# Optimization experiments

Measured on AMD Instinct MI355X. Metric: run time of the kernel, lower is better.

The kernel has to match this reference:

```python
import jax, jax.numpy as jnp
import numpy as np

DIM = 192
HEADS = 4
HID = int(DIM * 2.66)  # 510, Restormer GDFN hidden dim
EPS_LN = 1e-6


def ln2d(x, w, b):
    # torch LayerNorm2d variant: global mean/std over (C,H,W), std is UNBIASED (ddof=1)
    n = x.shape[1] * x.shape[2] * x.shape[3]
    mean = x.mean(axis=(1, 2, 3), keepdims=True)
    var = ((x - mean) ** 2).sum(axis=(1, 2, 3), keepdims=True) / (n - 1)
    return (x - mean) / (jnp.sqrt(var) + EPS_LN) * w + b


def conv1x1(x, w):
    # w: [O, C]; pointwise conv as channel matmul
    return jnp.einsum('bchw,oc->bohw', x, w)


def dwconv3(x, w):
    # w: [C, 1, 3, 3] depthwise 3x3, padding=1
    return jax.lax.conv_general_dilated(
        x, w, window_strides=(1, 1), padding='SAME',
        dimension_numbers=('NCHW', 'OIHW', 'NCHW'),
        feature_group_count=x.shape[1])


def setup_inputs() -> dict:
    key = jax.random.key(0)
    ks = jax.random.split(key, 8)
    s = 0.02
    return {
        'x': jax.random.normal(ks[0], (2, DIM, 256, 256), dtype=jnp.float32),
        'n1_w': jnp.ones((1, DIM, 1, 1), jnp.float32),
        'n1_b': jnp.zeros((1, DIM, 1, 1), jnp.float32),
        'qkv_w': jax.random.normal(ks[1], (3 * DIM, DIM), jnp.float32) * s,
        'qkv_dw_w': jax.random.normal(ks[2], (3 * DIM, 1, 3, 3), jnp.float32) * s,
        'proj_w': jax.random.normal(ks[3], (DIM, DIM), jnp.float32) * s,
        'temperature': jnp.ones((HEADS, 1, 1), jnp.float32),
        'n2_w': jnp.ones((1, DIM, 1, 1), jnp.float32),
        'n2_b': jnp.zeros((1, DIM, 1, 1), jnp.float32),
        'ff_in_w': jax.random.normal(ks[4], (2 * HID, DIM), jnp.float32) * s,
        'ff_dw_w': jax.random.normal(ks[5], (2 * HID, 1, 3, 3), jnp.float32) * s,
        'ff_out_w': jax.random.normal(ks[6], (DIM, HID), jnp.float32) * s,
    }


def reference(x, n1_w, n1_b, qkv_w, qkv_dw_w, proj_w, temperature,
              n2_w, n2_b, ff_in_w, ff_dw_w, ff_out_w):
    b, c, h, w = x.shape
    hd = c // HEADS

    # ---- MDTA attention ----
    y = ln2d(x, n1_w, n1_b)
    qkv = dwconv3(conv1x1(y, qkv_w), qkv_dw_w)  # [b, 3c, h, w]
    q, k, v = jnp.split(qkv, 3, axis=1)
    q = q.reshape(b, HEADS, hd, h * w)
    k = k.reshape(b, HEADS, hd, h * w)
    v = v.reshape(b, HEADS, hd, h * w)
    # L2-normalize along spatial axis (F.normalize, eps=1e-12)
    q = q / jnp.maximum(jnp.linalg.norm(q, axis=-1, keepdims=True), 1e-12)
    k = k / jnp.maximum(jnp.linalg.norm(k, axis=-1, keepdims=True), 1e-12)
    attn = jnp.einsum('bhcn,bhdn->bhcd', q, k) * temperature  # [b,H,hd,hd]
    attn = jax.nn.softmax(attn, axis=-1)
    out = jnp.einsum('bhcd,bhdn->bhcn', attn, v).reshape(b, c, h, w)
    x = x + conv1x1(out, proj_w)

    # ---- GDFN feed-forward ----
    y = ln2d(x, n2_w, n2_b)
    y = dwconv3(conv1x1(y, ff_in_w), ff_dw_w)  # [b, 2*HID, h, w]
    x1, x2 = jnp.split(y, 2, axis=1)
    y = jax.nn.gelu(x1, approximate=False) * x2
    x = x + conv1x1(y, ff_out_w)
    return x
```

## Files before the change

kernel.cpp:

```cpp
#include <hip/hip_runtime.h>
#include <hip/hip_bf16.h>

typedef unsigned short u16;
typedef __attribute__((ext_vector_type(8))) short short8;
typedef __attribute__((ext_vector_type(8))) unsigned short ushort8v;
typedef __attribute__((ext_vector_type(4))) float f32x4;

#define NPIX  65536
#define HH    256
#define WW    256
#define BATCH 2
#define CDIM  192
#define NHEADS 4
#define HD    48
#define OQKV  576
#define HIDN  510
#define OPAD  1024
#define NSLOT 32

__device__ __forceinline__ float bf2f(u16 b) {
  union { unsigned u; float f; } v; v.u = ((unsigned)b) << 16; return v.f;
}
__device__ __forceinline__ u16 f2bf(float f) {
  __bf16 h = (__bf16)f;
  u16 r; __builtin_memcpy(&r, &h, 2); return r;
}
__device__ __forceinline__ void atomAddF(float* p, float v) { unsafeAtomicAdd(p, v); }
__device__ __forceinline__ void gload16(const void* g, void* l) {
  __builtin_amdgcn_global_load_lds((const __attribute__((address_space(1))) unsigned int*)g,
                                   (__attribute__((address_space(3))) unsigned int*)l, 16, 0, 0);
}
__device__ __forceinline__ void xcdswz(int& bx, int& by) {
  const int nx = gridDim.x;
  const int tot = nx * gridDim.y;
  const int lin = by * nx + bx;
  const int q = tot >> 3, r = tot & 7;
  const int xcd = lin & 7, pos = lin >> 3;
  const int nl = (xcd < r) ? (xcd * (q + 1) + pos) : (r * (q + 1) + (xcd - r) * q + pos);
  bx = nl % nx; by = nl / nx;
}
__device__ __forceinline__ void dw3row(const u16* __restrict__ rp, int jm, bool hasL, bool hasR,
                                       float w0, float w1, float w2, float* acc) {
  ushort8v m = *(const ushort8v*)(rp + jm);
  float f[10];
  f[0] = hasL ? bf2f(rp[jm - 1]) : 0.f;
  #pragma unroll
  for (int t = 0; t < 8; ++t) f[t + 1] = bf2f(m[t]);
  f[9] = hasR ? bf2f(rp[jm + 8]) : 0.f;
  #pragma unroll
  for (int i = 0; i < 8; ++i) acc[i] += w0 * f[i] + w1 * f[i + 1] + w2 * f[i + 2];
}

#define OFF_STATS1 ((size_t)0)
#define OFF_STATS2 ((size_t)512)
#define OFF_G      ((size_t)1024)
#define OFF_NQ     (OFF_G + 2359296)
#define OFF_NK     (OFF_NQ + 49152)
#define ZERO_BYTES (OFF_NK + 49152)
#define OFF_BQ     ZERO_BYTES
#define OFF_B2     (OFF_BQ + 4608)
#define OFF_M      (OFF_B2 + 8192)
#define OFF_WQ     (OFF_M + 294912)
#define OFF_W2B    (OFF_WQ + 442368)
#define OFF_W3     (OFF_W2B + 786432)
#define OFF_T      (OFF_W3 + 196608)
#define OFF_QKV    (OFF_T + 50331648)
#define OFF_BAND   (OFF_QKV + 150994944)

__global__ __launch_bounds__(256) void k_statsT(const float* __restrict__ P, u16* __restrict__ T,
                                                float* __restrict__ stats) {
  __shared__ u16 ld[128][200];
  const int b = blockIdx.y, n0 = blockIdx.x * 128, tid = threadIdx.x;
  const int slot = blockIdx.x & (NSLOT - 1);
  const float* Pb = P + (((size_t)b * CDIM) << 16) + n0;
  float s = 0.f, ss = 0.f;
  for (int it = 0; it < 24; ++it) {
    int idx = it * 256 + tid;
    int c = idx >> 5, j = idx & 31;
    float4 v = *(const float4*)(Pb + ((size_t)c << 16) + j * 4);
    s  += v.x + v.y + v.z + v.w;
    ss += v.x*v.x + v.y*v.y + v.z*v.z + v.w*v.w;
    int px = j * 4;
    ld[px][c] = f2bf(v.x); ld[px+1][c] = f2bf(v.y);
    ld[px+2][c] = f2bf(v.z); ld[px+3][c] = f2bf(v.w);
  }
  for (int off = 32; off; off >>= 1) { s += __shfl_down(s, off); ss += __shfl_down(ss, off); }
  __shared__ float ls[4], lss[4];
  const int wid = tid >> 6, lane = tid & 63;
  if (lane == 0) { ls[wid] = s; lss[wid] = ss; }
  __syncthreads();
  if (tid == 0) {
    atomAddF(&stats[(slot * BATCH + b) * 2 + 0], ls[0]+ls[1]+ls[2]+ls[3]);
    atomAddF(&stats[(slot * BATCH + b) * 2 + 1], lss[0]+lss[1]+lss[2]+lss[3]);
  }
  u16* Tb = T + (size_t)(b * NPIX + n0) * CDIM;
  for (int it = 0; it < 12; ++it) {
    int idx = it * 256 + tid;
    int ch = idx % 24, nl = idx / 24;
    union { u16 s[8]; uint4 v; } t;
    #pragma unroll
    for (int r = 0; r < 8; ++r) t.s[r] = ld[nl][ch * 8 + r];
    int sch = ch ^ (nl & 7);
    *(uint4*)((char*)(Tb + (size_t)nl * CDIM) + sch * 16) = t.v;
  }
}

__global__ void k_fold(const float* __restrict__ w_in, const float* __restrict__ ln_w,
                       const float* __restrict__ ln_b, const float* __restrict__ stats,
                       u16* __restrict__ W, float* __restrict__ bias, int O_real) {
  const int o = blockIdx.x, b = blockIdx.y, c = threadIdx.x;
  const int Mtot = gridDim.x;
  const float n = (float)(CDIM * NPIX);
  float sum = 0.f, sumsq = 0.f;
  for (int sl = 0; sl < NSLOT; ++sl) {
    sum   += stats[(sl * BATCH + b) * 2 + 0];
    sumsq += stats[(sl * BATCH + b) * 2 + 1];
  }
  const float mean = sum / n;
  const float var = (sumsq - sum * sum / n) / (n - 1.f);
  const float inv = 1.f / (sqrtf(var) + 1e-6f);
  float we = 0.f, cb = 0.f;
  if (o < O_real) {
    float wi = w_in[o * CDIM + c];
    float a  = ln_w[c] * inv;
    we = wi * a;
    cb = wi * (ln_b[c] - mean * a);
  }
  int sch = (c >> 3) ^ (o & 7);
  W[((size_t)b * Mtot + o) * CDIM + sch * 8 + (c & 7)] = f2bf(we);
  for (int off = 32; off; off >>= 1) cb += __shfl_down(cb, off);
  __shared__ float l[3];
  if ((threadIdx.x & 63) == 0) l[threadIdx.x >> 6] = cb;
  __syncthreads();
  if (threadIdx.x == 0) bias[b * Mtot + o] = l[0] + l[1] + l[2];
}

__global__ void k_fold3(const float* __restrict__ w, u16* __restrict__ W3) {
  const int o = blockIdx.x;
  for (int it = 0; it < 2; ++it) {
    int c = it * 256 + threadIdx.x;
    float v = (c < HIDN) ? w[o * HIDN + c] : 0.f;
    int sch = (c >> 3) ^ (o & 7);
    W3[o * 512 + sch * 8 + (c & 7)] = f2bf(v);
  }
}

template <int KTOT, int KC, int EPI, int STATS, int NT>
__global__ __launch_bounds__(256) void k_mgemm(
    const u16* __restrict__ Bm, const u16* __restrict__ Am,
    const float* __restrict__ bias,
    const u16* __restrict__ rT, long rTbstr,
    void* __restrict__ outv, long Obstr, int out_nstr,
    u16* __restrict__ tout, long toutbstr,
    int Mtot, long Bbstr, long Abstr,
    int nB_base, int nB_rows, int nO_base, float* __restrict__ stats)
{
  constexpr int RBC = KC * 2;
  constexpr int NFR = NT / 64;
  constexpr int LDSB = (NT + 64) * KC * 2;
  constexpr int EPIB = (EPI == 0) ? 64 * (NT + 8) * 2
                     : (EPI == 2) ? 128 * 66 * 4
                     : ((EPI == 3) ? 128 * 66 * 2 : 0);
  constexpr int TOT  = LDSB > EPIB ? LDSB : EPIB;
  __shared__ char lds[TOT];
  u16* lB = (u16*)lds;
  u16* lA = (u16*)(lds + NT * KC * 2);
  const int b = blockIdx.z;
  int bx = blockIdx.x, by = blockIdx.y;
  xcdswz(bx, by);
  const int o0 = bx * 64;
  const int nB = nB_base + by * NT;
  const int nO = nO_base + by * NT;
  const int tid = threadIdx.x;
  const int lane = tid & 63;
  const int wid = tid >> 6;

  if (EPI == 0 && (nB < 0 || nB >= nB_rows)) {
    u16* op = (u16*)outv;
    uint4 z; z.x = z.y = z.z = z.w = 0u;
    constexpr int CH8 = NT / 8;
    #pragma unroll
    for (int it = 0; it < NT / 32; ++it) {
      int idx = it * 256 + tid;
      int orow = idx / CH8, c8 = idx % CH8;
      *(uint4*)(op + (size_t)b * Obstr + (size_t)(o0 + orow) * out_nstr + nO + c8 * 8) = z;
    }
    return;
  }

  const u16* Bb = Bm + (size_t)b * Bbstr + (size_t)nB * KTOT;
  const u16* Ab = Am + (size_t)b * Abstr + (size_t)o0 * KTOT;

  f32x4 acc[4][NFR];
  #pragma unroll
  for (int m = 0; m < 4; ++m)
    #pragma unroll
    for (int nf = 0; nf < NFR; ++nf) acc[m][nf] = (f32x4){0.f, 0.f, 0.f, 0.f};

  for (int kc0 = 0; kc0 < KTOT; kc0 += KC) {
    if (kc0) __syncthreads();
    constexpr int NCH = KC / 8;
    #pragma unroll
    for (int it = 0; it < NT * NCH / 256; ++it) {
      int idx = it * 256 + tid; int r = idx / NCH, ch = idx % NCH;
      gload16((const char*)(Bb + (size_t)r * KTOT + kc0) + ch * 16, (char*)lB + idx * 16);
    }
    #pragma unroll
    for (int it = 0; it < 64 * NCH / 256; ++it) {
      int idx = it * 256 + tid; int r = idx / NCH, ch = idx % NCH;
      gload16((const char*)(Ab + (size_t)r * KTOT + kc0) + ch * 16, (char*)lA + idx * 16);
    }
    __syncthreads();
    const int lr = lane & 15, g = lane >> 4;
    #pragma unroll
    for (int ks = 0; ks < KC / 32; ++ks) {
      const int ck = ks * 4 + g;
      short8 afr[4], bfr[NFR];
      #pragma unroll
      for (int m = 0; m < 4; ++m) {
        int row = m * 16 + lr;
        afr[m] = *(const short8*)((const char*)lA + row * RBC + ((ck ^ (row & 7)) << 4));
      }
      #pragma unroll
      for (int nf = 0; nf < NFR; ++nf) {
        int row = wid * (NT / 4) + nf * 16 + lr;
        bfr[nf] = *(const short8*)((const char*)lB + row * RBC + ((ck ^ (row & 7)) << 4));
      }
      #pragma unroll
      for (int m = 0; m < 4; ++m)
        #pragma unroll
        for (int nf = 0; nf < NFR; ++nf)
          acc[m][nf] = __builtin_amdgcn_mfma_f32_16x16x32_bf16(afr[m], bfr[nf], acc[m][nf], 0, 0, 0);
    }
  }

  const int col = lane & 15, rg = lane >> 4;
  if constexpr (EPI == 0) {
    constexpr int NTP = NT + 8;
    u16* lst = (u16*)lds;
    __syncthreads();
    #pragma unroll
    for (int m = 0; m < 4; ++m)
      #pragma unroll
      for (int j = 0; j < 4; ++j) {
        int r = m * 16 + rg * 4 + j;
        float bv = bias[b * Mtot + o0 + r];
        #pragma unroll
        for (int nf = 0; nf < NFR; ++nf) {
          int nn = wid * (NT / 4) + nf * 16 + col;
          lst[r * NTP + nn] = f2bf(acc[m][nf][j] + bv);
        }
      }
    __syncthreads();
    u16* op = (u16*)outv;
    constexpr int CH8 = NT / 8;
    #pragma unroll
    for (int it = 0; it < 64 * CH8 / 256; ++it) {
      int idx = it * 256 + tid;
      int r = idx / CH8, ch = idx % CH8;
      uint4 v = *(const uint4*)(lst + r * NTP + ch * 8);
      *(uint4*)(op + (size_t)b * Obstr + (size_t)(o0 + r) * out_nstr + nO + ch * 8) = v;
    }
  } else if constexpr (EPI == 2) {
    float* lBf = (float*)lds;
    __syncthreads();
    #pragma unroll
    for (int m = 0; m < 4; ++m)
      #pragma unroll
      for (int nf = 0; nf < NFR; ++nf)
        #pragma unroll
        for (int j = 0; j < 4; ++j)
          lBf[(wid * 32 + nf * 16 + col) * 66 + m * 16 + rg * 4 + j] = acc[m][nf][j];
    __syncthreads();
    float s = 0.f, ss = 0.f;
    for (int it = 0; it < 4; ++it) {
      int idx = it * 256 + tid;
      int n = idx >> 3, ch3 = idx & 7;
      size_t rowoff = (size_t)(nO + n) * CDIM;
      int chunk = (o0 >> 3) + (ch3 ^ (n & 7));
      uint4 xv = *(const uint4*)((const char*)(rT + (size_t)b * rTbstr + rowoff) + chunk * 16);
      u16* xs = (u16*)&xv;
      union { u16 s[8]; uint4 v; } t;
      #pragma unroll
      for (int r = 0; r < 8; ++r) {
        float rv = bf2f(xs[r]) + lBf[n * 66 + ch3 * 8 + r];
        t.s[r] = f2bf(rv);
        if constexpr (STATS) { s += rv; ss += rv * rv; }
      }
      *(uint4*)((char*)(tout + (size_t)b * toutbstr + rowoff) + chunk * 16) = t.v;
    }
    if constexpr (STATS) {
      for (int off = 32; off; off >>= 1) { s += __shfl_down(s, off); ss += __shfl_down(ss, off); }
      __shared__ float sr1[4], sr2[4];
      if (lane == 0) { sr1[wid] = s; sr2[wid] = ss; }
      __syncthreads();
      if (tid == 0) {
        int slot = by & (NSLOT - 1);
        atomAddF(&stats[(slot * BATCH + b) * 2 + 0], sr1[0]+sr1[1]+sr1[2]+sr1[3]);
        atomAddF(&stats[(slot * BATCH + b) * 2 + 1], sr2[0]+sr2[1]+sr2[2]+sr2[3]);
      }
    }
  } else {
    u16* lAx = (u16*)lds;
    __syncthreads();
    for (int it = 0; it < 4; ++it) {
      int idx = it * 256 + tid;
      int n = idx >> 3, ch3 = idx & 7;
      int chunk = (o0 >> 3) + (ch3 ^ (n & 7));
      uint4 xv = *(const uint4*)((const char*)(rT + (size_t)b * rTbstr + (size_t)(nO + n) * CDIM) + chunk * 16);
      u16* xs = (u16*)&xv;
      #pragma unroll
      for (int r = 0; r < 8; ++r) lAx[n * 66 + ch3 * 8 + r] = xs[r];
    }
    __syncthreads();
    float* of = (float*)outv;
    #pragma unroll
    for (int m = 0; m < 4; ++m)
      #pragma unroll
      for (int nf = 0; nf < NFR; ++nf)
        #pragma unroll
        for (int j = 0; j < 4; ++j) {
          int o = o0 + m * 16 + rg * 4 + j;
          int nl = wid * 32 + nf * 16 + col;
          size_t ix = (size_t)b * Obstr + (size_t)o * out_nstr + nO + nl;
          of[ix] = acc[m][nf][j] + bf2f(lAx[nl * 66 + m * 16 + rg * 4 + j]);
        }
  }
}

__global__ __launch_bounds__(256) void k_gram(const u16* __restrict__ qkv,
                                              const float* __restrict__ dww,
                                              float* __restrict__ G,
                                              float* __restrict__ nq,
                                              float* __restrict__ nk) {
  __shared__ u16 qs[HD][128], ks2[HD][128];
  __shared__ u16 wq[HD][9], wk[HD][9];
  __shared__ float nql[HD], nkl[HD];
  int bx = blockIdx.x, by = blockIdx.y;
  xcdswz(bx, by);
  const int b = by >> 2, h = by & 3;
  const int row = bx >> 1, col0 = (bx & 1) * 128;
  const int slot = bx & (NSLOT - 1);
  const int bh = b * NHEADS + h;
  const int tid = threadIdx.x;

  for (int idx = tid; idx < HD * 9; idx += 256) {
    int c = idx / 9, k9 = idx % 9;
    wq[c][k9] = f2bf(dww[(h * HD + c) * 9 + k9]);
    wk[c][k9] = f2bf(dww[(CDIM + h * HD + c) * 9 + k9]);
  }
  __syncthreads();

  for (int it = 0; it < 6; ++it) {
    int idx = it * 256 + tid;
    int j = idx & 15, cz = idx >> 4;
    int c = cz % HD, qk = cz / HD;
    const u16* base = qkv + (((size_t)(b * OQKV + qk * CDIM + h * HD + c)) << 16);
    const u16* w = qk ? wk[c] : wq[c];
    float acc[8] = {0.f,0.f,0.f,0.f,0.f,0.f,0.f,0.f};
    const int jm = col0 + j * 8;
    const bool hasL = jm > 0, hasR = jm < 248;
    if (row > 0)   dw3row(base + (row - 1) * 256, jm, hasL, hasR, bf2f(w[0]), bf2f(w[1]), bf2f(w[2]), acc);
                   dw3row(base + row * 256,       jm, hasL, hasR, bf2f(w[3]), bf2f(w[4]), bf2f(w[5]), acc);
    if (row < 255) dw3row(base + (row + 1) * 256, jm, hasL, hasR, bf2f(w[6]), bf2f(w[7]), bf2f(w[8]), acc);
    union { u16 s[8]; ushort8v v; } rv;
    float sqs = 0.f;
    #pragma unroll
    for (int i = 0; i < 8; ++i) {
      rv.s[i] = f2bf(acc[i]);
      sqs += acc[i] * acc[i];
    }
    const int sw = (j ^ (c & 7)) * 8;
    if (qk) *(ushort8v*)&ks2[c][sw] = rv.v;
    else    *(ushort8v*)&qs[c][sw]  = rv.v;
    sqs += __shfl_down(sqs, 8);
    sqs += __shfl_down(sqs, 4);
    sqs += __shfl_down(sqs, 2);
    sqs += __shfl_down(sqs, 1);
    if ((tid & 15) == 0) { if (qk) nkl[c] = sqs; else nql[c] = sqs; }
  }
  __syncthreads();

  if (tid < HD) atomAddF(&nq[(slot * 2 * NHEADS + bh) * HD + tid], nql[tid]);
  else if (tid < 2*HD) atomAddF(&nk[(slot * 2 * NHEADS + bh) * HD + tid - HD], nkl[tid - HD]);

  const int lane = tid & 63, wid = tid >> 6;
  const int lr = lane & 15, g = lane >> 4;
  float* Gb = G + (size_t)(slot * 2 * NHEADS + bh) * HD * HD;
  for (int t = wid; t < 9; t += 4) {
    const int m = t / 3, nb = t % 3;
    f32x4 a4 = (f32x4){0.f, 0.f, 0.f, 0.f};
    #pragma unroll
    for (int ksi = 0; ksi < 4; ++ksi) {
      int ck = ksi * 4 + g;
      int ra = m * 16 + lr, rb = nb * 16 + lr;
      short8 af = *(const short8*)&qs[ra][(ck ^ (ra & 7)) * 8];
      short8 bf = *(const short8*)&ks2[rb][(ck ^ (rb & 7)) * 8];
      a4 = __builtin_amdgcn_mfma_f32_16x16x32_bf16(af, bf, a4, 0, 0, 0);
    }
    #pragma unroll
    for (int jj = 0; jj < 4; ++jj)
      atomAddF(&Gb[(m * 16 + g * 4 + jj) * HD + nb * 16 + lr], a4[jj]);
  }
}

__global__ void k_attnM(const float* __restrict__ G, const float* __restrict__ nq,
                        const float* __restrict__ nk, const float* __restrict__ temp,
                        const float* __restrict__ proj_w, u16* __restrict__ Mb16) {
  const int h = blockIdx.x, b = blockIdx.y;
  const int bh = b * NHEADS + h;
  __shared__ float at[HD][HD];
  __shared__ float nqs[HD], nks[HD];
  const int tid = threadIdx.x;
  if (tid < HD) {
    float s = 0.f;
    for (int sl = 0; sl < NSLOT; ++sl) s += nq[(sl * 2 * NHEADS + bh) * HD + tid];
    nqs[tid] = fmaxf(sqrtf(s), 1e-12f);
  } else if (tid >= 64 && tid < 64 + HD) {
    int c = tid - 64;
    float s = 0.f;
    for (int sl = 0; sl < NSLOT; ++sl) s += nk[(sl * 2 * NHEADS + bh) * HD + c];
    nks[c] = fmaxf(sqrtf(s), 1e-12f);
  }
  __syncthreads();
  const float t = temp[h];
  for (int idx = tid; idx < HD * HD; idx += 256) {
    int c = idx / HD, d = idx % HD;
    float g = 0.f;
    for (int sl = 0; sl < NSLOT; ++sl)
      g += G[(size_t)(sl * 2 * NHEADS + bh) * HD * HD + idx];
    at[c][d] = g / (nqs[c] * nks[d]) * t;
  }
  __syncthreads();
  if (tid < HD) {
    float m = -1e30f;
    for (int d = 0; d < HD; ++d) m = fmaxf(m, at[tid][d]);
    float s = 0.f;
    for (int d = 0; d < HD; ++d) { float e = __expf(at[tid][d] - m); at[tid][d] = e; s += e; }
    float inv = 1.f / s;
    for (int d = 0; d < HD; ++d) at[tid][d] *= inv;
  }
  __syncthreads();
  for (int idx = tid; idx < CDIM * HD; idx += 256) {
    int o = idx / HD, d = idx % HD;
    float acc = 0.f;
    for (int c = 0; c < HD; ++c) acc += proj_w[o * CDIM + h * HD + c] * at[c][d];
    int cf = h * HD + d;
    int sch = (cf >> 3) ^ (o & 7);
    Mb16[((size_t)(b * CDIM + o)) * CDIM + sch * 8 + (cf & 7)] = f2bf(acc);
  }
}

__global__ __launch_bounds__(256) void k_dwT(const u16* __restrict__ qkv,
                                             const float* __restrict__ dww,
                                             u16* __restrict__ vdwT, long vdwbstr) {
  __shared__ u16 ld[64][201];
  __shared__ float w9[CDIM][9];
  int bx = blockIdx.x, by = blockIdx.y;
  xcdswz(bx, by);
  const int b = by;
  const int p0 = bx * 64;
  const int row = p0 >> 8, col0 = p0 & 255;
  const int tid = threadIdx.x;
  for (int idx = tid; idx < CDIM * 9; idx += 256) w9[idx / 9][idx % 9] = dww[384 * 9 + idx];
  __syncthreads();
  for (int it = 0; it < 6; ++it) {
    int idx = it * 256 + tid;
    int j = idx & 7, c = idx >> 3;
    const u16* base = qkv + (((size_t)(b * OQKV + 384 + c)) << 16);
    const float* w = w9[c];
    float acc[8] = {0.f,0.f,0.f,0.f,0.f,0.f,0.f,0.f};
    const int jm = col0 + j * 8;
    const bool hasL = jm > 0, hasR = jm < 248;
    if (row > 0)   dw3row(base + (row - 1) * 256, jm, hasL, hasR, w[0], w[1], w[2], acc);
                   dw3row(base + row * 256,       jm, hasL, hasR, w[3], w[4], w[5], acc);
    if (row < 255) dw3row(base + (row + 1) * 256, jm, hasL, hasR, w[6], w[7], w[8], acc);
    #pragma unroll
    for (int i = 0; i < 8; ++i) ld[j * 8 + i][c] = f2bf(acc[i]);
  }
  __syncthreads();
  u16* Tb = vdwT + (size_t)b * vdwbstr + (size_t)p0 * CDIM;
  for (int it = 0; it < 6; ++it) {
    int idx = it * 256 + tid;
    int ch = idx % 24, pl = idx / 24;
    union { u16 s[8]; uint4 v; } t;
    #pragma unroll
    for (int r = 0; r < 8; ++r) t.s[r] = ld[pl][ch * 8 + r];
    int sch = ch ^ (pl & 7);
    *(uint4*)((char*)(Tb + (size_t)pl * CDIM) + sch * 16) = t.v;
  }
}

__global__ __launch_bounds__(256) void k_dwgT(const u16* __restrict__ hp_, const float* __restrict__ w9,
                                              u16* __restrict__ ygT, int rows_loc, int band_px) {
  __shared__ u16 ld[32][515];
  int bx = blockIdx.x, by = blockIdx.y;
  xcdswz(bx, by);
  const int b = by;
  const int p0 = bx * 32;
  const int olr = p0 >> 8, col0 = p0 & 255;
  const int tid = threadIdx.x;
  if (tid < 64) {
    int px = tid >> 1, c = 510 + (tid & 1);
    ld[px][c] = 0;
  }
  __syncthreads();
  for (int it = 0; it < 8; ++it) {
    int idx = it * 256 + tid;
    if (idx >= HIDN * 4) break;
    int j = idx & 3, c = idx >> 2;
    const u16* ia = hp_ + (size_t)(b * OPAD + c) * rows_loc * 256;
    const u16* ig = hp_ + (size_t)(b * OPAD + c + HIDN) * rows_loc * 256;
    float aa[8] = {0.f,0.f,0.f,0.f,0.f,0.f,0.f,0.f};
    float gg[8] = {0.f,0.f,0.f,0.f,0.f,0.f,0.f,0.f};
    const int jm = col0 + j * 8;
    const bool hasL = jm > 0, hasR = jm < 248;
    #pragma unroll
    for (int dr = 0; dr < 3; ++dr) {
      dw3row(ia + (olr + dr) * 256, jm, hasL, hasR,
             w9[c * 9 + dr * 3], w9[c * 9 + dr * 3 + 1], w9[c * 9 + dr * 3 + 2], aa);
      dw3row(ig + (olr + dr) * 256, jm, hasL, hasR,
             w9[(c + HIDN) * 9 + dr * 3], w9[(c + HIDN) * 9 + dr * 3 + 1],
             w9[(c + HIDN) * 9 + dr * 3 + 2], gg);
    }
    #pragma unroll
    for (int i = 0; i < 8; ++i) {
      float a = aa[i];
      float gel = 0.5f * a * (1.f + erff(a * 0.70710678118654752f));
      ld[j * 8 + i][c] = f2bf(gel * gg[i]);
    }
  }
  __syncthreads();
  u16* Tb = ygT + ((size_t)b * band_px + p0) * 512;
  for (int it = 0; it < 8; ++it) {
    int idx = it * 256 + tid;
    int ch = idx & 63, pl = idx >> 6;
    union { u16 s[8]; uint4 v; } t;
    #pragma unroll
    for (int r = 0; r < 8; ++r) t.s[r] = ld[pl][ch * 8 + r];
    int sch = ch ^ (pl & 7);
    *(uint4*)((char*)(Tb + (size_t)pl * 512) + sch * 16) = t.v;
  }
}

extern "C" void kernel_launch(void* const* d_in, const int* in_sizes, int n_in,
                              void* d_out, int out_size, void* d_ws, size_t ws_size,
                              hipStream_t stream) {
  const float* x       = (const float*)d_in[0];
  const float* n1_w    = (const float*)d_in[1];
  const float* n1_b    = (const float*)d_in[2];
  const float* qkv_w   = (const float*)d_in[3];
  const float* qkv_dw  = (const float*)d_in[4];
  const float* proj_w  = (const float*)d_in[5];
  const float* temp    = (const float*)d_in[6];
  const float* n2_w    = (const float*)d_in[7];
  const float* n2_b    = (const float*)d_in[8];
  const float* ff_in_w = (const float*)d_in[9];
  const float* ff_dw   = (const float*)d_in[10];
  const float* ff_out_w= (const float*)d_in[11];

  char* ws = (char*)d_ws;
  float* stats1 = (float*)(ws + OFF_STATS1);
  float* stats2 = (float*)(ws + OFF_STATS2);
  float* G      = (float*)(ws + OFF_G);
  float* nq     = (float*)(ws + OFF_NQ);
  float* nk     = (float*)(ws + OFF_NK);
  float* biasq  = (float*)(ws + OFF_BQ);
  float* bias2  = (float*)(ws + OFF_B2);
  u16*   Mb16   = (u16*)(ws + OFF_M);
  u16*   Wq     = (u16*)(ws + OFF_WQ);
  u16*   W2b    = (u16*)(ws + OFF_W2B);
  u16*   W3     = (u16*)(ws + OFF_W3);
  u16*   xT     = (u16*)(ws + OFF_T);
  u16*   qkv    = (u16*)(ws + OFF_QKV);
  u16*   vdwT   = qkv;
  u16*   x2T    = qkv + (size_t)CDIM * NPIX;
  const long qkvbstr = (long)OQKV * NPIX;
  float* outp   = (float*)d_out;

  int NP = 32;
  const int cand[4] = {2, 4, 8, 16};
  for (int i = 0; i < 4; ++i) {
    int rws = 256 / cand[i], rl = rws + 2;
    size_t band = (size_t)2 * OPAD * rl * 256 * 2 + (size_t)2 * rws * 256 * 512 * 2;
    if (OFF_BAND + band + ((size_t)8 << 20) <= ws_size) { NP = cand[i]; break; }
  }
  const int rows = 256 / NP, rows_loc = rows + 2, band_px = rows * 256;
  u16* hpre = (u16*)(ws + OFF_BAND);
  u16* ygT  = (u16*)(ws + OFF_BAND + (size_t)2 * OPAD * rows_loc * 256 * 2);

  hipMemsetAsync(ws, 0, ZERO_BYTES, stream);

  k_statsT<<<dim3(NPIX / 128, BATCH), 256, 0, stream>>>(x, xT, stats1);
  k_fold<<<dim3(OQKV, BATCH), CDIM, 0, stream>>>(qkv_w, n1_w, n1_b, stats1, Wq, biasq, OQKV);
  k_mgemm<192, 64, 0, 0, 256><<<dim3(OQKV / 64, NPIX / 256, BATCH), 256, 0, stream>>>(
      xT, Wq, biasq, nullptr, 0L, qkv, (long)OQKV * NPIX, NPIX, nullptr, 0L,
      OQKV, (long)NPIX * CDIM, (long)OQKV * CDIM, 0, NPIX, 0, nullptr);
  k_gram<<<dim3(512, BATCH * NHEADS), 256, 0, stream>>>(qkv, qkv_dw, G, nq, nk);
  k_attnM<<<dim3(NHEADS, BATCH), 256, 0, stream>>>(G, nq, nk, temp, proj_w, Mb16);
  k_dwT<<<dim3(NPIX / 64, BATCH), 256, 0, stream>>>(qkv, qkv_dw, vdwT, qkvbstr);
  k_mgemm<192, 64, 2, 1, 128><<<dim3(CDIM / 64, NPIX / 128, BATCH), 256, 0, stream>>>(
      vdwT, Mb16, nullptr, xT, (long)NPIX * CDIM, nullptr, 0L, 0, x2T, qkvbstr,
      CDIM, qkvbstr, (long)CDIM * CDIM, 0, NPIX, 0, stats2);

  k_fold<<<dim3(OPAD, BATCH), CDIM, 0, stream>>>(ff_in_w, n2_w, n2_b, stats2, W2b, bias2, 1020);
  k_fold3<<<dim3(CDIM), 256, 0, stream>>>(ff_out_w, W3);
  for (int rp = 0; rp < NP; ++rp) {
    const int band0 = rp * band_px;
    k_mgemm<192, 64, 0, 0, 256><<<dim3(OPAD / 64, rows_loc, BATCH), 256, 0, stream>>>(
        x2T, W2b, bias2, nullptr, 0L, hpre, (long)OPAD * rows_loc * 256, rows_loc * 256,
        nullptr, 0L, OPAD, qkvbstr, (long)OPAD * CDIM, band0 - 256, NPIX, 0, nullptr);
    k_dwgT<<<dim3(band_px / 32, BATCH), 256, 0, stream>>>(hpre, ff_dw, ygT, rows_loc, band_px);
    k_mgemm<512, 128, 3, 0, 128><<<dim3(CDIM / 64, rows * 2, BATCH), 256, 0, stream>>>(
        ygT, W3, nullptr, x2T, qkvbstr, outp, (long)CDIM * NPIX, NPIX, nullptr, 0L,
        CDIM, (long)band_px * 512, 0L, 0, band_px, band0, nullptr);
  }
}
```

Baseline: 750.4 us.

## Halve per-block tiles in depthwise/gram kernels and coalesce final GEMM stores

The final output GEMM epilogue now stages residual-added fp32 results through LDS, then writes them as coalesced float4 rows instead of scattered scalar stores. k_gram, k_dwT and k_dwgT each process half as many pixels per block, and twice as many blocks are launched, to raise occupancy and parallelism. k_gram uses a shorter K loop, and k_dwT stores its weights as bf16 in LDS. The costs are an extra LDS round trip and barriers in the epilogue, more per-block overhead, and twice as many atomic adds into the gram slots.

```diff
diff --git a/kernel.cpp b/kernel.cpp
--- a/kernel.cpp
+++ b/kernel.cpp
@@ -160,7 +160,7 @@
   constexpr int LDSB = (NT + 64) * KC * 2;
   constexpr int EPIB = (EPI == 0) ? 64 * (NT + 8) * 2
                      : (EPI == 2) ? 128 * 66 * 4
-                     : ((EPI == 3) ? 128 * 66 * 2 : 0);
+                     : ((EPI == 3) ? 64 * 132 * 4 : 0);
   constexpr int TOT  = LDSB > EPIB ? LDSB : EPIB;
   __shared__ char lds[TOT];
   u16* lB = (u16*)lds;
@@ -313,18 +313,33 @@
       for (int r = 0; r < 8; ++r) lAx[n * 66 + ch3 * 8 + r] = xs[r];
     }
     __syncthreads();
-    float* of = (float*)outv;
     #pragma unroll
     for (int m = 0; m < 4; ++m)
       #pragma unroll
       for (int nf = 0; nf < NFR; ++nf)
         #pragma unroll
         for (int j = 0; j < 4; ++j) {
-          int o = o0 + m * 16 + rg * 4 + j;
           int nl = wid * 32 + nf * 16 + col;
-          size_t ix = (size_t)b * Obstr + (size_t)o * out_nstr + nO + nl;
-          of[ix] = acc[m][nf][j] + bf2f(lAx[nl * 66 + m * 16 + rg * 4 + j]);
+          acc[m][nf][j] += bf2f(lAx[nl * 66 + m * 16 + rg * 4 + j]);
         }
+    __syncthreads();
+    float* lstf = (float*)lds;
+    #pragma unroll
+    for (int m = 0; m < 4; ++m)
+      #pragma unroll
+      for (int nf = 0; nf < NFR; ++nf)
+        #pragma unroll
+        for (int j = 0; j < 4; ++j)
+          lstf[(m * 16 + rg * 4 + j) * 132 + wid * 32 + nf * 16 + col] = acc[m][nf][j];
+    __syncthreads();
+    float* of = (float*)outv;
+    #pragma unroll
+    for (int it = 0; it < 8; ++it) {
+      int idx = it * 256 + tid;
+      int r = idx >> 5, q4 = idx & 31;
+      float4 v = *(const float4*)&lstf[r * 132 + q4 * 4];
+      *(float4*)(of + (size_t)b * Obstr + (size_t)(o0 + r) * out_nstr + nO + q4 * 4) = v;
+    }
   }
 }
 
@@ -333,13 +348,13 @@
                                               float* __restrict__ G,
                                               float* __restrict__ nq,
                                               float* __restrict__ nk) {
-  __shared__ u16 qs[HD][128], ks2[HD][128];
+  __shared__ u16 qs[HD][64], ks2[HD][64];
   __shared__ u16 wq[HD][9], wk[HD][9];
   __shared__ float nql[HD], nkl[HD];
   int bx = blockIdx.x, by = blockIdx.y;
   xcdswz(bx, by);
   const int b = by >> 2, h = by & 3;
-  const int row = bx >> 1, col0 = (bx & 1) * 128;
+  const int row = bx >> 2, col0 = (bx & 3) * 64;
   const int slot = bx & (NSLOT - 1);
   const int bh = b * NHEADS + h;
   const int tid = threadIdx.x;
@@ -351,9 +366,9 @@
   }
   __syncthreads();
 
-  for (int it = 0; it < 6; ++it) {
+  for (int it = 0; it < 3; ++it) {
     int idx = it * 256 + tid;
-    int j = idx & 15, cz = idx >> 4;
+    int j = idx & 7, cz = idx >> 3;
     int c = cz % HD, qk = cz / HD;
     const u16* base = qkv + (((size_t)(b * OQKV + qk * CDIM + h * HD + c)) << 16);
     const u16* w = qk ? wk[c] : wq[c];
@@ -373,11 +388,10 @@
     const int sw = (j ^ (c & 7)) * 8;
     if (qk) *(ushort8v*)&ks2[c][sw] = rv.v;
     else    *(ushort8v*)&qs[c][sw]  = rv.v;
-    sqs += __shfl_down(sqs, 8);
     sqs += __shfl_down(sqs, 4);
     sqs += __shfl_down(sqs, 2);
     sqs += __shfl_down(sqs, 1);
-    if ((tid & 15) == 0) { if (qk) nkl[c] = sqs; else nql[c] = sqs; }
+    if ((tid & 7) == 0) { if (qk) nkl[c] = sqs; else nql[c] = sqs; }
   }
   __syncthreads();
 
@@ -391,7 +405,7 @@
     const int m = t / 3, nb = t % 3;
     f32x4 a4 = (f32x4){0.f, 0.f, 0.f, 0.f};
     #pragma unroll
-    for (int ksi = 0; ksi < 4; ++ksi) {
+    for (int ksi = 0; ksi < 2; ++ksi) {
       int ck = ksi * 4 + g;
       int ra = m * 16 + lr, rb = nb * 16 + lr;
       short8 af = *(const short8*)&qs[ra][(ck ^ (ra & 7)) * 8];
@@ -454,61 +468,61 @@
 __global__ __launch_bounds__(256) void k_dwT(const u16* __restrict__ qkv,
                                              const float* __restrict__ dww,
                                              u16* __restrict__ vdwT, long vdwbstr) {
-  __shared__ u16 ld[64][201];
-  __shared__ float w9[CDIM][9];
-  int bx = blockIdx.x, by = blockIdx.y;
-  xcdswz(bx, by);
-  const int b = by;
-  const int p0 = bx * 64;
-  const int row = p0 >> 8, col0 = p0 & 255;
-  const int tid = threadIdx.x;
-  for (int idx = tid; idx < CDIM * 9; idx += 256) w9[idx / 9][idx % 9] = dww[384 * 9 + idx];
-  __syncthreads();
-  for (int it = 0; it < 6; ++it) {
-    int idx = it * 256 + tid;
-    int j = idx & 7, c = idx >> 3;
-    const u16* base = qkv + (((size_t)(b * OQKV + 384 + c)) << 16);
-    const float* w = w9[c];
-    float acc[8] = {0.f,0.f,0.f,0.f,0.f,0.f,0.f,0.f};
-    const int jm = col0 + j * 8;
-    const bool hasL = jm > 0, hasR = jm < 248;
-    if (row > 0)   dw3row(base + (row - 1) * 256, jm, hasL, hasR, w[0], w[1], w[2], acc);
-                   dw3row(base + row * 256,       jm, hasL, hasR, w[3], w[4], w[5], acc);
-    if (row < 255) dw3row(base + (row + 1) * 256, jm, hasL, hasR, w[6], w[7], w[8], acc);
-    #pragma unroll
-    for (int i = 0; i < 8; ++i) ld[j * 8 + i][c] = f2bf(acc[i]);
-  }
-  __syncthreads();
-  u16* Tb = vdwT + (size_t)b * vdwbstr + (size_t)p0 * CDIM;
-  for (int it = 0; it < 6; ++it) {
-    int idx = it * 256 + tid;
-    int ch = idx % 24, pl = idx / 24;
-    union { u16 s[8]; uint4 v; } t;
-    #pragma unroll
-    for (int r = 0; r < 8; ++r) t.s[r] = ld[pl][ch * 8 + r];
-    int sch = ch ^ (pl & 7);
-    *(uint4*)((char*)(Tb + (size_t)pl * CDIM) + sch * 16) = t.v;
-  }
-}
-
-__global__ __launch_bounds__(256) void k_dwgT(const u16* __restrict__ hp_, const float* __restrict__ w9,
-                                              u16* __restrict__ ygT, int rows_loc, int band_px) {
-  __shared__ u16 ld[32][515];
+  __shared__ u16 ld[32][201];
+  __shared__ u16 w9[CDIM][9];
   int bx = blockIdx.x, by = blockIdx.y;
   xcdswz(bx, by);
   const int b = by;
   const int p0 = bx * 32;
+  const int row = p0 >> 8, col0 = p0 & 255;
+  const int tid = threadIdx.x;
+  for (int idx = tid; idx < CDIM * 9; idx += 256) w9[idx / 9][idx % 9] = f2bf(dww[384 * 9 + idx]);
+  __syncthreads();
+  for (int it = 0; it < 3; ++it) {
+    int idx = it * 256 + tid;
+    int j = idx & 3, c = idx >> 2;
+    const u16* base = qkv + (((size_t)(b * OQKV + 384 + c)) << 16);
+    const u16* w = w9[c];
+    float acc[8] = {0.f,0.f,0.f,0.f,0.f,0.f,0.f,0.f};
+    const int jm = col0 + j * 8;
+    const bool hasL = jm > 0, hasR = jm < 248;
+    if (row > 0)   dw3row(base + (row - 1) * 256, jm, hasL, hasR, bf2f(w[0]), bf2f(w[1]), bf2f(w[2]), acc);
+                   dw3row(base + row * 256,       jm, hasL, hasR, bf2f(w[3]), bf2f(w[4]), bf2f(w[5]), acc);
+    if (row < 255) dw3row(base + (row + 1) * 256, jm, hasL, hasR, bf2f(w[6]), bf2f(w[7]), bf2f(w[8]), acc);
+    #pragma unroll
+    for (int i = 0; i < 8; ++i) ld[j * 8 + i][c] = f2bf(acc[i]);
+  }
+  __syncthreads();
+  u16* Tb = vdwT + (size_t)b * vdwbstr + (size_t)p0 * CDIM;
+  for (int it = 0; it < 3; ++it) {
+    int idx = it * 256 + tid;
+    int ch = idx % 24, pl = idx / 24;
+    union { u16 s[8]; uint4 v; } t;
+    #pragma unroll
+    for (int r = 0; r < 8; ++r) t.s[r] = ld[pl][ch * 8 + r];
+    int sch = ch ^ (pl & 7);
+    *(uint4*)((char*)(Tb + (size_t)pl * CDIM) + sch * 16) = t.v;
+  }
+}
+
+__global__ __launch_bounds__(256) void k_dwgT(const u16* __restrict__ hp_, const float* __restrict__ w9,
+                                              u16* __restrict__ ygT, int rows_loc, int band_px) {
+  __shared__ u16 ld[16][515];
+  int bx = blockIdx.x, by = blockIdx.y;
+  xcdswz(bx, by);
+  const int b = by;
+  const int p0 = bx * 16;
   const int olr = p0 >> 8, col0 = p0 & 255;
   const int tid = threadIdx.x;
-  if (tid < 64) {
+  if (tid < 32) {
     int px = tid >> 1, c = 510 + (tid & 1);
     ld[px][c] = 0;
   }
   __syncthreads();
-  for (int it = 0; it < 8; ++it) {
+  for (int it = 0; it < 4; ++it) {
     int idx = it * 256 + tid;
-    if (idx >= HIDN * 4) break;
-    int j = idx & 3, c = idx >> 2;
+    if (idx >= HIDN * 2) break;
+    int j = idx & 1, c = idx >> 1;
     const u16* ia = hp_ + (size_t)(b * OPAD + c) * rows_loc * 256;
     const u16* ig = hp_ + (size_t)(b * OPAD + c + HIDN) * rows_loc * 256;
     float aa[8] = {0.f,0.f,0.f,0.f,0.f,0.f,0.f,0.f};
@@ -532,7 +546,7 @@
   }
   __syncthreads();
   u16* Tb = ygT + ((size_t)b * band_px + p0) * 512;
-  for (int it = 0; it < 8; ++it) {
+  for (int it = 0; it < 4; ++it) {
     int idx = it * 256 + tid;
     int ch = idx & 63, pl = idx >> 6;
     union { u16 s[8]; uint4 v; } t;
@@ -596,9 +610,9 @@
   k_mgemm<192, 64, 0, 0, 256><<<dim3(OQKV / 64, NPIX / 256, BATCH), 256, 0, stream>>>(
       xT, Wq, biasq, nullptr, 0L, qkv, (long)OQKV * NPIX, NPIX, nullptr, 0L,
       OQKV, (long)NPIX * CDIM, (long)OQKV * CDIM, 0, NPIX, 0, nullptr);
-  k_gram<<<dim3(512, BATCH * NHEADS), 256, 0, stream>>>(qkv, qkv_dw, G, nq, nk);
+  k_gram<<<dim3(1024, BATCH * NHEADS), 256, 0, stream>>>(qkv, qkv_dw, G, nq, nk);
   k_attnM<<<dim3(NHEADS, BATCH), 256, 0, stream>>>(G, nq, nk, temp, proj_w, Mb16);
-  k_dwT<<<dim3(NPIX / 64, BATCH), 256, 0, stream>>>(qkv, qkv_dw, vdwT, qkvbstr);
+  k_dwT<<<dim3(NPIX / 32, BATCH), 256, 0, stream>>>(qkv, qkv_dw, vdwT, qkvbstr);
   k_mgemm<192, 64, 2, 1, 128><<<dim3(CDIM / 64, NPIX / 128, BATCH), 256, 0, stream>>>(
       vdwT, Mb16, nullptr, xT, (long)NPIX * CDIM, nullptr, 0L, 0, x2T, qkvbstr,
       CDIM, qkvbstr, (long)CDIM * CDIM, 0, NPIX, 0, stats2);
@@ -610,7 +624,7 @@
     k_mgemm<192, 64, 0, 0, 256><<<dim3(OPAD / 64, rows_loc, BATCH), 256, 0, stream>>>(
         x2T, W2b, bias2, nullptr, 0L, hpre, (long)OPAD * rows_loc * 256, rows_loc * 256,
         nullptr, 0L, OPAD, qkvbstr, (long)OPAD * CDIM, band0 - 256, NPIX, 0, nullptr);
-    k_dwgT<<<dim3(band_px / 32, BATCH), 256, 0, stream>>>(hpre, ff_dw, ygT, rows_loc, band_px);
+    k_dwgT<<<dim3(band_px / 16, BATCH), 256, 0, stream>>>(hpre, ff_dw, ygT, rows_loc, band_px);
     k_mgemm<512, 128, 3, 0, 128><<<dim3(CDIM / 64, rows * 2, BATCH), 256, 0, stream>>>(
         ygT, W3, nullptr, x2T, qkvbstr, outp, (long)CDIM * NPIX, NPIX, nullptr, 0L,
         CDIM, (long)band_px * 512, 0L, 0, band_px, band0, nullptr);
```

Result: slower. 876.6 us (+16.8%).
